# Optimization experiments

Hardware: AMD Instinct MI355X
Metric: run time of the kernel (lower is better)

The kernel has to match this reference:

```python
import jax, jax.numpy as jnp
import numpy as np

C = 3.0e8
WAVE_LAMBDA = 0.0038
PI = float(np.pi)


def _grid(size, resolution, x_val):
    edge_left = [-i for i in range(1, size, 2)][::-1]
    edge_right = [i for i in range(1, size, 2)]
    edge = edge_left + edge_right
    if size % 2 == 1:
        edge = [i for i in range(-(size - 1), size, 2)]
    edge = np.array(edge, dtype=np.float32) * resolution / 2.0
    wx, wy = np.meshgrid(edge, edge)
    wz = np.zeros((size, size), dtype=np.float32)
    pos = np.stack((wz, wx, wy), 2).reshape(size * size, 3).astype(np.float32)
    pos[:, 0] = x_val
    return pos


def setup_inputs() -> dict:
    key = jax.random.key(0)
    k1, k2, k3 = jax.random.split(key, 3)
    lam = WAVE_LAMBDA
    f = np.arange(77e9, 81e9 + 1e9, 1e9, dtype=np.float32)  # [5]
    tx = np.array([[0, -8 * lam, 0], [0, -6 * lam, 0], [0, -4 * lam, 0], [0, -2 * lam, 0],
                   [0, 0, 0], [0, 2 * lam, 0], [0, 4 * lam, 0], [0, 6 * lam, 0], [0, 8 * lam, 0],
                   [0, -2.5 * lam, -3 * lam], [0, -3.0 * lam, -2 * lam], [0, -3.5 * lam, -0.5 * lam]],
                  dtype=np.float32)  # [12,3]
    rx = np.array([[0, -16 * lam, -0.066], [0, -15.5 * lam, -0.066], [0, -15 * lam, -0.066],
                   [0, -14.5 * lam, -0.066], [0, -10.5 * lam, -0.066], [0, -10 * lam, -0.066],
                   [0, -9.5 * lam, -0.066], [0, -9 * lam, -0.066], [0, 7 * lam, -0.066],
                   [0, 7.5 * lam, -0.066], [0, 8 * lam, -0.066], [0, 8.5 * lam, -0.066],
                   [0, 9 * lam, -0.066], [0, 9.5 * lam, -0.066], [0, 10 * lam, -0.066],
                   [0, 10.5 * lam, -0.066]], dtype=np.float32)  # [16,3]
    meta = _grid(60, 0.0015, 0.1)     # [3600,3]
    scene = _grid(20, 0.0015, 0.3)    # [400,3] (resolution reassigned to 0.0015 in torch init)
    # trainable params
    meta_theta = jax.random.uniform(k1, (3600, 1), jnp.float32,
                                    minval=-PI, maxval=20 * PI / 180.0)
    w = jax.random.normal(k2, (5, 6, 12), jnp.float32)
    T = jax.random.normal(k3, (400, 128), jnp.float32)
    return {"T": T, "w": w, "meta_theta": meta_theta, "f": jnp.asarray(f),
            "tx_positions": jnp.asarray(tx), "rx_positions": jnp.asarray(rx),
            "meta_positions": jnp.asarray(meta), "scene_positions": jnp.asarray(scene)}


def _channel(locs_start, locs_end, f):
    # pairwise distance [Ns,Ne], then complex channel [F,Ns,Ne]
    d = jnp.linalg.norm(locs_start[:, None, :] - locs_end[None, :, :], axis=2)
    return (0.001 / d ** 2) * jnp.exp(-1j * 2 * PI * f[:, None, None] * d / C)


def reference(T, w, meta_theta, f, tx_positions, rx_positions, meta_positions, scene_positions):
    theta = jnp.clip(meta_theta, -PI, 20 * PI / 180.0)[:, 0]   # [M]
    phase = jnp.exp(1j * theta)                                # [M]
    pri = jnp.exp(1j * w)                                      # [F,6,Tx]
    H1 = _channel(tx_positions, meta_positions, f)             # [F,Tx,M]
    H2 = _channel(meta_positions, scene_positions, f)          # [F,M,S]
    H3 = _channel(scene_positions, meta_positions, f)          # [F,S,M]
    H4 = _channel(meta_positions, rx_positions, f)             # [F,M,Rx]
    A = jnp.einsum('fkt,ftm->fkm', pri, H1)                    # [F,6,M]
    A = A * phase[None, None, :]
    A = jnp.einsum('fkm,fms->fks', A, H2)                      # [F,6,S]
    # diag_embed(A) @ H3  ==  per-row scaling of H3 (no dense SxS diag needed)
    A = A[..., None] * H3[:, None, :, :]                       # [F,6,S,M]
    A = A * phase[None, None, None, :]
    A = jnp.einsum('fksm,fmr->fksr', A, H4)                    # [F,6,S,Rx]
    A = jnp.transpose(A, (3, 0, 1, 2))                         # [Rx,F,6,S]
    A = jnp.tile(A, (1, 1, 12, 1))                             # [Rx,F,72,S]
    A = A.reshape(-1, A.shape[3])                              # [Rx*F*72, S]
    T_complex = T.astype(jnp.complex64)
    mic_data = A @ T_complex                                   # [Rx*F*72, B]
    s_A = jnp.concatenate([A.real, A.imag], axis=0)            # [2*Rx*F*72, S]
    s_mic = jnp.concatenate([mic_data.real, mic_data.imag], axis=0)[..., None]
    return (s_A, s_mic)
```

## Files before the change

### kernel.cpp

```cpp
#include <hip/hip_runtime.h>
#include <hip/hip_bf16.h>
#include <math.h>

#define F_N 5
#define K_N 6
#define T_N 12
#define M_N 3600
#define S_N 400
#define R_N 16
#define B_N 128

#define PI_F 3.14159265358979f
#define CLIP_HI 0.3490658503988659f
#define NEG_TWO_PI_OVER_C (-6.283185307179586f / 3.0e8f)

#define SA_BASE   0
#define MIC_BASE  4608000

#define NK 113
#define KP (NK * 32)
#define W_ELEMS  (5 * 48 * KP)
#define H_ELEMS  (5 * 800 * KP)
#define C_ELEMS  (4 * 5 * 48 * 800)
#define WS_NEED  ((size_t)(W_ELEMS + H_ELEMS) * 2 + (size_t)C_ELEMS * 4)

typedef __attribute__((ext_vector_type(8))) short bf16x8;
typedef __attribute__((ext_vector_type(4))) float f32x4;

__device__ __forceinline__ void fast_sincos(float x, float* s, float* c) {
    float r = x * 0.15915494309189535f;
    r -= floorf(r);
    *s = __builtin_amdgcn_sinf(r);
    *c = __builtin_amdgcn_cosf(r);
}


__global__ __launch_bounds__(256) void stage_kernel(
    const float* __restrict__ w, const float* __restrict__ meta_theta,
    const float* __restrict__ fin, const float* __restrict__ txp,
    const float* __restrict__ rxp, const float* __restrict__ metap,
    const float* __restrict__ scenep,
    __hip_bfloat16* __restrict__ Wbf, __hip_bfloat16* __restrict__ Hbf)
{
    const int tid = threadIdx.x;
    const int blk = blockIdx.x;

    if (blk < 75) {
        __shared__ float pri[K_N * T_N * 2];
        __shared__ float txs[T_N * 3];
        __shared__ float rxs[R_N * 3];
        const int f = blk / 15;
        const int mblk = blk % 15;

        if (tid < K_N * T_N) {
            float sv, cv; fast_sincos(w[f * (K_N * T_N) + tid], &sv, &cv);
            pri[tid * 2] = cv; pri[tid * 2 + 1] = sv;
        }
        if (tid >= 64 && tid < 64 + T_N * 3) txs[tid - 64] = txp[tid - 64];
        if (tid >= 128 && tid < 128 + R_N * 3) rxs[tid - 128] = rxp[tid - 128];
        __syncthreads();

        const int m = mblk * 256 + tid;
        if (m >= KP) return;
        __hip_bfloat16* wb = Wbf + ((size_t)(f * NK + (m >> 5)) * 48) * 32 + (m & 31);

        if (m >= M_N) {
            for (int row = 0; row < 48; ++row) wb[row * 32] = __float2bfloat16(0.f);
            return;
        }

        const float px = metap[m * 3 + 0];
        const float py = metap[m * 3 + 1];
        const float pz = metap[m * 3 + 2];
        const float coef = NEG_TWO_PI_OVER_C * fin[f];

        float th = meta_theta[m];
        th = fminf(fmaxf(th, -PI_F), CLIP_HI);
        float phs, phc; fast_sincos(th, &phs, &phc);

        float hre[T_N], him[T_N];
#pragma unroll
        for (int t = 0; t < T_N; ++t) {
            float dx = txs[t * 3 + 0] - px, dy = txs[t * 3 + 1] - py, dz = txs[t * 3 + 2] - pz;
            float d = sqrtf(dx * dx + dy * dy + dz * dz);
            float amp = 1e-3f / (d * d);
            float sv, cv; fast_sincos(coef * d, &sv, &cv);
            hre[t] = amp * cv; him[t] = amp * sv;
        }
#pragma unroll
        for (int k = 0; k < K_N; ++k) {
            float ar = 0.f, ai = 0.f;
#pragma unroll
            for (int t = 0; t < T_N; ++t) {
                float pr = pri[(k * T_N + t) * 2], pim = pri[(k * T_N + t) * 2 + 1];
                ar += pr * hre[t] - pim * him[t];
                ai += pr * him[t] + pim * hre[t];
            }
            wb[k * 32]        = __float2bfloat16(ar * phc - ai * phs);
            wb[(22 + k) * 32] = __float2bfloat16(ar * phs + ai * phc);
        }
#pragma unroll
        for (int r = 0; r < R_N; ++r) {
            float dx = rxs[r * 3 + 0] - px, dy = rxs[r * 3 + 1] - py, dz = rxs[r * 3 + 2] - pz;
            float d = sqrtf(dx * dx + dy * dy + dz * dz);
            float amp = 1e-3f / (d * d);
            float sv, cv; fast_sincos(coef * d, &sv, &cv);
            float cr = amp * cv, ci = amp * sv;
            wb[(6 + r) * 32]  = __float2bfloat16(cr * phc - ci * phs);
            wb[(28 + r) * 32] = __float2bfloat16(cr * phs + ci * phc);
        }
#pragma unroll
        for (int row = 44; row < 48; ++row) wb[row * 32] = __float2bfloat16(0.f);
    } else {
        const int q = blk - 75;
        const int f = q / S_N;
        const int s = q % S_N;
        const float coef = NEG_TWO_PI_OVER_C * fin[f];
        const float sx = scenep[s * 3 + 0];
        const float sy = scenep[s * 3 + 1];
        const float sz = scenep[s * 3 + 2];

        for (int m = tid; m < KP; m += 256) {
            float re = 0.f, im = 0.f;
            if (m < M_N) {
                float px = metap[m * 3 + 0], py = metap[m * 3 + 1], pz = metap[m * 3 + 2];
                float dx = px - sx, dy = py - sy, dz = pz - sz;
                float d = sqrtf(dx * dx + dy * dy + dz * dz);
                float amp = 1e-3f / (d * d);
                float sv, cv; fast_sincos(coef * d, &sv, &cv);
                re = amp * cv; im = amp * sv;
            }
            size_t idx = ((size_t)(f * NK + (m >> 5)) * 800 + s) * 32 + (m & 31);
            Hbf[idx] = __float2bfloat16(re);
            Hbf[idx + 400 * 32] = __float2bfloat16(im);
        }
    }
}

__global__ __launch_bounds__(128) void gemm_kernel(
    const ushort* __restrict__ Wbf, const ushort* __restrict__ Hbf,
    float* __restrict__ Cp)
{
    const int blk = blockIdx.x;
    const int f = blk / 100;
    const int rem = blk % 100;
    const int nblk = rem / 4;
    const int ksp = rem % 4;
    const int wave = threadIdx.x >> 6;
    const int lane = threadIdx.x & 63;
    const int quad = lane >> 4;
    const int l16 = lane & 15;

    const int n = nblk * 32 + wave * 16 + l16;
    const int kbeg = (ksp == 0) ? 0 : (29 + 28 * (ksp - 1));
    const int kcnt = (ksp == 0) ? 29 : 28;

    f32x4 acc0 = {0.f, 0.f, 0.f, 0.f};
    f32x4 acc1 = {0.f, 0.f, 0.f, 0.f};
    f32x4 acc2 = {0.f, 0.f, 0.f, 0.f};

    for (int kk = 0; kk < kcnt; ++kk) {
        const int kb = kbeg + kk;
        bf16x8 b  = *(const bf16x8*)(Hbf + ((size_t)(f * NK + kb) * 800 + n) * 32 + quad * 8);
        const ushort* wbase = Wbf + ((size_t)(f * NK + kb) * 48) * 32 + quad * 8;
        bf16x8 a0 = *(const bf16x8*)(wbase + (size_t)l16 * 32);
        bf16x8 a1 = *(const bf16x8*)(wbase + (size_t)(16 + l16) * 32);
        bf16x8 a2 = *(const bf16x8*)(wbase + (size_t)(32 + l16) * 32);
        acc0 = __builtin_amdgcn_mfma_f32_16x16x32_bf16(a0, b, acc0, 0, 0, 0);
        acc1 = __builtin_amdgcn_mfma_f32_16x16x32_bf16(a1, b, acc1, 0, 0, 0);
        acc2 = __builtin_amdgcn_mfma_f32_16x16x32_bf16(a2, b, acc2, 0, 0, 0);
    }

    float* cb = Cp + ((size_t)(ksp * 5 + f) * 48) * 800;
#pragma unroll
    for (int i = 0; i < 4; ++i) {
        int row = quad * 4 + i;
        cb[(size_t)row * 800 + n]        = acc0[i];
        cb[(size_t)(16 + row) * 800 + n] = acc1[i];
        cb[(size_t)(32 + row) * 800 + n] = acc2[i];
    }
}

__device__ __forceinline__ void combineC(const float* __restrict__ Cp, int f, int row,
                                         int s, float* re, float* im) {
    float r = 0.f, i = 0.f;
#pragma unroll
    for (int p = 0; p < 4; ++p) {
        const float* c = Cp + ((size_t)(p * 5 + f) * 48) * 800;
        r += c[(size_t)row * 800 + s]       - c[(size_t)(22 + row) * 800 + 400 + s];
        i += c[(size_t)row * 800 + 400 + s] + c[(size_t)(22 + row) * 800 + s];
    }
    *re = r; *im = i;
}

#define SA_BLOCKS 750
__global__ __launch_bounds__(256) void epilogue2_kernel(
    const float* __restrict__ Cp, const float* __restrict__ T,
    float* __restrict__ out)
{
    __shared__ float cre[S_N], cim[S_N];
    __shared__ float pR[256], pI[256];
    const int tid = threadIdx.x;
    const int blk = blockIdx.x;

    if (blk < SA_BLOCKS) {
        int i = blk * 256 + tid;
        int s = i % S_N; int rest = i / S_N;
        int k = rest % K_N; rest /= K_N;
        int f = rest % F_N; int r = rest / F_N;

        float ar, ai, br, bi;
        combineC(Cp, f, k, s, &ar, &ai);
        combineC(Cp, f, 6 + r, s, &br, &bi);
        float cr = ar * br - ai * bi;
        float ci = ar * bi + ai * br;

        int base = (r * F_N + f) * 72;
#pragma unroll
        for (int j = 0; j < 12; ++j) {
            int row = base + j * K_N + k;
            out[SA_BASE + (size_t)row * S_N + s] = cr;
            out[SA_BASE + (size_t)(5760 + row) * S_N + s] = ci;
        }
    } else {
        int bk = blk - SA_BLOCKS;
        int k = bk % K_N;
        int f = (bk / K_N) % F_N;
        int r = bk / (K_N * F_N);

        for (int s = tid; s < S_N; s += 256) {
            float ar, ai, br, bi;
            combineC(Cp, f, k, s, &ar, &ai);
            combineC(Cp, f, 6 + r, s, &br, &bi);
            cre[s] = ar * br - ai * bi;
            cim[s] = ar * bi + ai * br;
        }
        __syncthreads();

        const int b = tid & 127;
        const int hs = tid >> 7;
        float accR = 0.f, accI = 0.f;
        const int sBeg = hs * 200, sEnd = sBeg + 200;
#pragma unroll 4
        for (int s = sBeg; s < sEnd; ++s) {
            float tv = T[s * B_N + b];
            accR += cre[s] * tv;
            accI += cim[s] * tv;
        }
        pR[tid] = accR; pI[tid] = accI;
        __syncthreads();
        if (tid < 128) {
            accR = pR[tid] + pR[tid + 128];
            accI = pI[tid] + pI[tid + 128];
            int base = (r * F_N + f) * 72;
#pragma unroll
            for (int j = 0; j < 12; ++j) {
                int row = base + j * K_N + k;
                out[MIC_BASE + (size_t)row * B_N + b] = accR;
                out[MIC_BASE + (size_t)(5760 + row) * B_N + b] = accI;
            }
        }
    }
}

__global__ __launch_bounds__(256) void prep_kernel(
    const float* __restrict__ w, const float* __restrict__ meta_theta,
    const float* __restrict__ fin, const float* __restrict__ txp,
    const float* __restrict__ rxp, const float* __restrict__ metap,
    float* __restrict__ A1, float* __restrict__ H4p)
{
    __shared__ float pri[K_N * T_N * 2];
    __shared__ float txs[T_N * 3];
    __shared__ float rxs[R_N * 3];
    const int tid = threadIdx.x;
    const int f = blockIdx.x / 15;
    const int mblk = blockIdx.x % 15;

    if (tid < K_N * T_N) {
        float sv, cv; fast_sincos(w[f * (K_N * T_N) + tid], &sv, &cv);
        pri[tid * 2] = cv; pri[tid * 2 + 1] = sv;
    }
    if (tid >= 64 && tid < 64 + T_N * 3) txs[tid - 64] = txp[tid - 64];
    if (tid >= 128 && tid < 128 + R_N * 3) rxs[tid - 128] = rxp[tid - 128];
    __syncthreads();

    const int m = mblk * 256 + tid;
    if (m >= M_N) return;

    const float px = metap[m * 3 + 0];
    const float py = metap[m * 3 + 1];
    const float pz = metap[m * 3 + 2];
    const float coef = NEG_TWO_PI_OVER_C * fin[f];

    float th = meta_theta[m];
    th = fminf(fmaxf(th, -PI_F), CLIP_HI);
    float phs, phc; fast_sincos(th, &phs, &phc);

    float hre[T_N], him[T_N];
#pragma unroll
    for (int t = 0; t < T_N; ++t) {
        float dx = txs[t * 3 + 0] - px, dy = txs[t * 3 + 1] - py, dz = txs[t * 3 + 2] - pz;
        float d = sqrtf(dx * dx + dy * dy + dz * dz);
        float amp = 1e-3f / (d * d);
        float sv, cv; fast_sincos(coef * d, &sv, &cv);
        hre[t] = amp * cv; him[t] = amp * sv;
    }
    float* a1 = A1 + ((size_t)f * M_N + m) * (K_N * 2);
#pragma unroll
    for (int k = 0; k < K_N; ++k) {
        float ar = 0.f, ai = 0.f;
#pragma unroll
        for (int t = 0; t < T_N; ++t) {
            float pr = pri[(k * T_N + t) * 2], pim = pri[(k * T_N + t) * 2 + 1];
            ar += pr * hre[t] - pim * him[t];
            ai += pr * him[t] + pim * hre[t];
        }
        a1[k * 2]     = ar * phc - ai * phs;
        a1[k * 2 + 1] = ar * phs + ai * phc;
    }
    float* h4 = H4p + ((size_t)f * M_N + m) * (R_N * 2);
#pragma unroll
    for (int r = 0; r < R_N; ++r) {
        float dx = rxs[r * 3 + 0] - px, dy = rxs[r * 3 + 1] - py, dz = rxs[r * 3 + 2] - pz;
        float d = sqrtf(dx * dx + dy * dy + dz * dz);
        float amp = 1e-3f / (d * d);
        float sv, cv; fast_sincos(coef * d, &sv, &cv);
        float cr = amp * cv, ci = amp * sv;
        h4[r * 2]     = cr * phc - ci * phs;
        h4[r * 2 + 1] = cr * phs + ci * phc;
    }
}

__global__ __launch_bounds__(256, 2) void main_kernel(
    const float* __restrict__ fin, const float* __restrict__ metap,
    const float* __restrict__ scenep, const float* __restrict__ A1,
    const float* __restrict__ H4p, float* __restrict__ A2, float* __restrict__ Bm)
{
    const int f = blockIdx.x / 200;
    const int sq = blockIdx.x % 200;
    const int s0 = 2 * sq, s1 = s0 + 1;
    const int tid = threadIdx.x;

    const float coef = NEG_TWO_PI_OVER_C * fin[f];
    const float sx0 = scenep[s0 * 3], sy0 = scenep[s0 * 3 + 1], sz0 = scenep[s0 * 3 + 2];
    const float sx1 = scenep[s1 * 3], sy1 = scenep[s1 * 3 + 1], sz1 = scenep[s1 * 3 + 2];

    float acc[88];
#pragma unroll
    for (int i = 0; i < 88; ++i) acc[i] = 0.f;

    const float4* a1base = (const float4*)(A1 + (size_t)f * M_N * (K_N * 2));
    const float4* h4base = (const float4*)(H4p + (size_t)f * M_N * (R_N * 2));

    for (int m = tid; m < M_N; m += 256) {
        float px = metap[m * 3 + 0], py = metap[m * 3 + 1], pz = metap[m * 3 + 2];
        float dx0 = px - sx0, dy0 = py - sy0, dz0 = pz - sz0;
        float d0 = sqrtf(dx0 * dx0 + dy0 * dy0 + dz0 * dz0);
        float dx1 = px - sx1, dy1 = py - sy1, dz1 = pz - sz1;
        float d1 = sqrtf(dx1 * dx1 + dy1 * dy1 + dz1 * dz1);
        float sv0, cv0, sv1, cv1;
        fast_sincos(coef * d0, &sv0, &cv0);
        fast_sincos(coef * d1, &sv1, &cv1);
        float amp0 = 1e-3f / (d0 * d0), amp1 = 1e-3f / (d1 * d1);
        float h2r0 = amp0 * cv0, h2i0 = amp0 * sv0;
        float h2r1 = amp1 * cv1, h2i1 = amp1 * sv1;

        const float4* a1 = a1base + (size_t)m * 3;
#pragma unroll
        for (int q = 0; q < 3; ++q) {
            float4 v = a1[q];
            acc[4 * q + 0] += v.x * h2r0 - v.y * h2i0;
            acc[4 * q + 1] += v.x * h2i0 + v.y * h2r0;
            acc[4 * q + 2] += v.z * h2r0 - v.w * h2i0;
            acc[4 * q + 3] += v.z * h2i0 + v.w * h2r0;
            acc[44 + 4 * q + 0] += v.x * h2r1 - v.y * h2i1;
            acc[44 + 4 * q + 1] += v.x * h2i1 + v.y * h2r1;
            acc[44 + 4 * q + 2] += v.z * h2r1 - v.w * h2i1;
            acc[44 + 4 * q + 3] += v.z * h2i1 + v.w * h2r1;
        }
        const float4* h4 = h4base + (size_t)m * 8;
#pragma unroll
        for (int q = 0; q < 8; ++q) {
            float4 v = h4[q];
            acc[12 + 4 * q + 0] += v.x * h2r0 - v.y * h2i0;
            acc[12 + 4 * q + 1] += v.x * h2i0 + v.y * h2r0;
            acc[12 + 4 * q + 2] += v.z * h2r0 - v.w * h2i0;
            acc[12 + 4 * q + 3] += v.z * h2i0 + v.w * h2r0;
            acc[56 + 4 * q + 0] += v.x * h2r1 - v.y * h2i1;
            acc[56 + 4 * q + 1] += v.x * h2i1 + v.y * h2r1;
            acc[56 + 4 * q + 2] += v.z * h2r1 - v.w * h2i1;
            acc[56 + 4 * q + 3] += v.z * h2i1 + v.w * h2r1;
        }
    }

#pragma unroll
    for (int off = 32; off > 0; off >>= 1) {
#pragma unroll
        for (int i = 0; i < 88; ++i) acc[i] += __shfl_down(acc[i], off);
    }
    __shared__ float red[4][88];
    const int wave = tid >> 6, lane = tid & 63;
    if (lane == 0) {
#pragma unroll
        for (int i = 0; i < 88; ++i) red[wave][i] = acc[i];
    }
    __syncthreads();
    if (tid < 88) {
        float v = red[0][tid] + red[1][tid] + red[2][tid] + red[3][tid];
        int half = tid / 44, slot = tid - 44 * half;
        int s = half ? s1 : s0;
        if (slot < 12) {
            int k = slot >> 1, c = slot & 1;
            A2[(((size_t)f * K_N + k) * S_N + s) * 2 + c] = v;
        } else {
            int j = slot - 12; int r = j >> 1, c = j & 1;
            Bm[(((size_t)f * S_N + s) * R_N + r) * 2 + c] = v;
        }
    }
}

__global__ __launch_bounds__(256) void epilogue_kernel(
    const float* __restrict__ A2, const float* __restrict__ Bm,
    const float* __restrict__ T, float* __restrict__ out)
{
    __shared__ float cre[S_N], cim[S_N];
    __shared__ float pR[256], pI[256];
    const int tid = threadIdx.x;
    const int blk = blockIdx.x;

    if (blk < SA_BLOCKS) {
        int i = blk * 256 + tid;
        int s = i % S_N; int rest = i / S_N;
        int k = rest % K_N; rest /= K_N;
        int f = rest % F_N; int r = rest / F_N;

        float ar = A2[((f * K_N + k) * S_N + s) * 2];
        float ai = A2[((f * K_N + k) * S_N + s) * 2 + 1];
        float br = Bm[((f * S_N + s) * R_N + r) * 2];
        float bi = Bm[((f * S_N + s) * R_N + r) * 2 + 1];
        float cr = ar * br - ai * bi;
        float ci = ar * bi + ai * br;

        int base = (r * F_N + f) * 72;
#pragma unroll
        for (int j = 0; j < 12; ++j) {
            int row = base + j * K_N + k;
            out[SA_BASE + (size_t)row * S_N + s] = cr;
            out[SA_BASE + (size_t)(5760 + row) * S_N + s] = ci;
        }
    } else {
        int bk = blk - SA_BLOCKS;
        int k = bk % K_N;
        int f = (bk / K_N) % F_N;
        int r = bk / (K_N * F_N);

        for (int s = tid; s < S_N; s += 256) {
            float ar = A2[((f * K_N + k) * S_N + s) * 2];
            float ai = A2[((f * K_N + k) * S_N + s) * 2 + 1];
            float br = Bm[((f * S_N + s) * R_N + r) * 2];
            float bi = Bm[((f * S_N + s) * R_N + r) * 2 + 1];
            cre[s] = ar * br - ai * bi;
            cim[s] = ar * bi + ai * br;
        }
        __syncthreads();

        const int b = tid & 127;
        const int hs = tid >> 7;
        float accR = 0.f, accI = 0.f;
        const int sBeg = hs * 200, sEnd = sBeg + 200;
#pragma unroll 4
        for (int s = sBeg; s < sEnd; ++s) {
            float tv = T[s * B_N + b];
            accR += cre[s] * tv;
            accI += cim[s] * tv;
        }
        pR[tid] = accR; pI[tid] = accI;
        __syncthreads();
        if (tid < 128) {
            accR = pR[tid] + pR[tid + 128];
            accI = pI[tid] + pI[tid + 128];
            int base = (r * F_N + f) * 72;
#pragma unroll
            for (int j = 0; j < 12; ++j) {
                int row = base + j * K_N + k;
                out[MIC_BASE + (size_t)row * B_N + b] = accR;
                out[MIC_BASE + (size_t)(5760 + row) * B_N + b] = accI;
            }
        }
    }
}

extern "C" void kernel_launch(void* const* d_in, const int* in_sizes, int n_in,
                              void* d_out, int out_size, void* d_ws, size_t ws_size,
                              hipStream_t stream) {
    const float* T  = (const float*)d_in[0];
    const float* w  = (const float*)d_in[1];
    const float* th = (const float*)d_in[2];
    const float* fr = (const float*)d_in[3];
    const float* tx = (const float*)d_in[4];
    const float* rx = (const float*)d_in[5];
    const float* mp = (const float*)d_in[6];
    const float* sp = (const float*)d_in[7];

    float* out = (float*)d_out;

    if (ws_size >= WS_NEED) {
        __hip_bfloat16* Wbf = (__hip_bfloat16*)d_ws;
        __hip_bfloat16* Hbf = Wbf + W_ELEMS;
        float* Cp = (float*)(Hbf + H_ELEMS);

        stage_kernel<<<75 + 2000, 256, 0, stream>>>(w, th, fr, tx, rx, mp, sp, Wbf, Hbf);
        gemm_kernel<<<500, 128, 0, stream>>>((const ushort*)Wbf, (const ushort*)Hbf, Cp);
        epilogue2_kernel<<<SA_BLOCKS + 480, 256, 0, stream>>>(Cp, T, out);
    } else {
        float* ws  = (float*)d_ws;
        float* A1  = ws;
        float* H4p = ws + 216000;
        float* A2  = ws + 792000;
        float* Bm  = ws + 816000;

        prep_kernel<<<75, 256, 0, stream>>>(w, th, fr, tx, rx, mp, A1, H4p);
        main_kernel<<<F_N * 200, 256, 0, stream>>>(fr, mp, sp, A1, H4p, A2, Bm);
        epilogue_kernel<<<SA_BLOCKS + 480, 256, 0, stream>>>(A2, Bm, T, out);
    }
}
```

Before: 122.8 us.

## Compute scene-meta channel on the fly inside GEMM instead of materializing it

The stage kernel no longer builds the bf16 H matrix (scene×meta channel, real and imaginary parts) in workspace. Instead, each GEMM lane computes its B-fragment values (distance, amplitude, sin or cos) directly from the positions before issuing the MFMAs. This removes roughly 2000 stage blocks and a large global write and read round-trip. In exchange the GEMM loop does transcendental math per element, and the real and imaginary halves each recompute the shared distance work. The GEMM grid is only 500 blocks, so compute latency may not be hidden.

```diff
diff --git a/kernel.cpp b/kernel.cpp
--- a/kernel.cpp
+++ b/kernel.cpp
@@ -13,6 +13,7 @@
 #define PI_F 3.14159265358979f
 #define CLIP_HI 0.3490658503988659f
 #define NEG_TWO_PI_OVER_C (-6.283185307179586f / 3.0e8f)
+#define INV_TWO_PI 0.15915494309189535f
 
 #define SA_BASE   0
 #define MIC_BASE  4608000
@@ -20,18 +21,23 @@
 #define NK 113
 #define KP (NK * 32)
 #define W_ELEMS  (5 * 48 * KP)
-#define H_ELEMS  (5 * 800 * KP)
 #define C_ELEMS  (4 * 5 * 48 * 800)
-#define WS_NEED  ((size_t)(W_ELEMS + H_ELEMS) * 2 + (size_t)C_ELEMS * 4)
+#define WS_NEED  ((size_t)W_ELEMS * 2 + (size_t)C_ELEMS * 4)
 
 typedef __attribute__((ext_vector_type(8))) short bf16x8;
 typedef __attribute__((ext_vector_type(4))) float f32x4;
 
 __device__ __forceinline__ void fast_sincos(float x, float* s, float* c) {
-    float r = x * 0.15915494309189535f;
+    float r = x * INV_TWO_PI;
     r -= floorf(r);
     *s = __builtin_amdgcn_sinf(r);
     *c = __builtin_amdgcn_cosf(r);
+}
+
+__device__ __forceinline__ ushort f2bf(float v) {
+    __hip_bfloat16 h = __float2bfloat16(v);
+    union { __hip_bfloat16 h; ushort u; } cv; cv.h = h;
+    return cv.u;
 }
 
 
@@ -39,106 +45,79 @@
     const float* __restrict__ w, const float* __restrict__ meta_theta,
     const float* __restrict__ fin, const float* __restrict__ txp,
     const float* __restrict__ rxp, const float* __restrict__ metap,
-    const float* __restrict__ scenep,
-    __hip_bfloat16* __restrict__ Wbf, __hip_bfloat16* __restrict__ Hbf)
+    __hip_bfloat16* __restrict__ Wbf)
 {
+    __shared__ float pri[K_N * T_N * 2];
+    __shared__ float txs[T_N * 3];
+    __shared__ float rxs[R_N * 3];
     const int tid = threadIdx.x;
-    const int blk = blockIdx.x;
-
-    if (blk < 75) {
-        __shared__ float pri[K_N * T_N * 2];
-        __shared__ float txs[T_N * 3];
-        __shared__ float rxs[R_N * 3];
-        const int f = blk / 15;
-        const int mblk = blk % 15;
-
-        if (tid < K_N * T_N) {
-            float sv, cv; fast_sincos(w[f * (K_N * T_N) + tid], &sv, &cv);
-            pri[tid * 2] = cv; pri[tid * 2 + 1] = sv;
-        }
-        if (tid >= 64 && tid < 64 + T_N * 3) txs[tid - 64] = txp[tid - 64];
-        if (tid >= 128 && tid < 128 + R_N * 3) rxs[tid - 128] = rxp[tid - 128];
-        __syncthreads();
-
-        const int m = mblk * 256 + tid;
-        if (m >= KP) return;
-        __hip_bfloat16* wb = Wbf + ((size_t)(f * NK + (m >> 5)) * 48) * 32 + (m & 31);
-
-        if (m >= M_N) {
-            for (int row = 0; row < 48; ++row) wb[row * 32] = __float2bfloat16(0.f);
-            return;
-        }
-
-        const float px = metap[m * 3 + 0];
-        const float py = metap[m * 3 + 1];
-        const float pz = metap[m * 3 + 2];
-        const float coef = NEG_TWO_PI_OVER_C * fin[f];
-
-        float th = meta_theta[m];
-        th = fminf(fmaxf(th, -PI_F), CLIP_HI);
-        float phs, phc; fast_sincos(th, &phs, &phc);
-
-        float hre[T_N], him[T_N];
+    const int f = blockIdx.x / 15;
+    const int mblk = blockIdx.x % 15;
+
+    if (tid < K_N * T_N) {
+        float sv, cv; fast_sincos(w[f * (K_N * T_N) + tid], &sv, &cv);
+        pri[tid * 2] = cv; pri[tid * 2 + 1] = sv;
+    }
+    if (tid >= 64 && tid < 64 + T_N * 3) txs[tid - 64] = txp[tid - 64];
+    if (tid >= 128 && tid < 128 + R_N * 3) rxs[tid - 128] = rxp[tid - 128];
+    __syncthreads();
+
+    const int m = mblk * 256 + tid;
+    if (m >= KP) return;
+    __hip_bfloat16* wb = Wbf + ((size_t)(f * NK + (m >> 5)) * 48) * 32 + (m & 31);
+
+    if (m >= M_N) {
+        for (int row = 0; row < 48; ++row) wb[row * 32] = __float2bfloat16(0.f);
+        return;
+    }
+
+    const float px = metap[m * 3 + 0];
+    const float py = metap[m * 3 + 1];
+    const float pz = metap[m * 3 + 2];
+    const float coef = NEG_TWO_PI_OVER_C * fin[f];
+
+    float th = meta_theta[m];
+    th = fminf(fmaxf(th, -PI_F), CLIP_HI);
+    float phs, phc; fast_sincos(th, &phs, &phc);
+
+    float hre[T_N], him[T_N];
+#pragma unroll
+    for (int t = 0; t < T_N; ++t) {
+        float dx = txs[t * 3 + 0] - px, dy = txs[t * 3 + 1] - py, dz = txs[t * 3 + 2] - pz;
+        float d = sqrtf(dx * dx + dy * dy + dz * dz);
+        float amp = 1e-3f / (d * d);
+        float sv, cv; fast_sincos(coef * d, &sv, &cv);
+        hre[t] = amp * cv; him[t] = amp * sv;
+    }
+#pragma unroll
+    for (int k = 0; k < K_N; ++k) {
+        float ar = 0.f, ai = 0.f;
 #pragma unroll
         for (int t = 0; t < T_N; ++t) {
-            float dx = txs[t * 3 + 0] - px, dy = txs[t * 3 + 1] - py, dz = txs[t * 3 + 2] - pz;
-            float d = sqrtf(dx * dx + dy * dy + dz * dz);
-            float amp = 1e-3f / (d * d);
-            float sv, cv; fast_sincos(coef * d, &sv, &cv);
-            hre[t] = amp * cv; him[t] = amp * sv;
-        }
-#pragma unroll
-        for (int k = 0; k < K_N; ++k) {
-            float ar = 0.f, ai = 0.f;
-#pragma unroll
-            for (int t = 0; t < T_N; ++t) {
-                float pr = pri[(k * T_N + t) * 2], pim = pri[(k * T_N + t) * 2 + 1];
-                ar += pr * hre[t] - pim * him[t];
-                ai += pr * him[t] + pim * hre[t];
-            }
-            wb[k * 32]        = __float2bfloat16(ar * phc - ai * phs);
-            wb[(22 + k) * 32] = __float2bfloat16(ar * phs + ai * phc);
-        }
-#pragma unroll
-        for (int r = 0; r < R_N; ++r) {
-            float dx = rxs[r * 3 + 0] - px, dy = rxs[r * 3 + 1] - py, dz = rxs[r * 3 + 2] - pz;
-            float d = sqrtf(dx * dx + dy * dy + dz * dz);
-            float amp = 1e-3f / (d * d);
-            float sv, cv; fast_sincos(coef * d, &sv, &cv);
-            float cr = amp * cv, ci = amp * sv;
-            wb[(6 + r) * 32]  = __float2bfloat16(cr * phc - ci * phs);
-            wb[(28 + r) * 32] = __float2bfloat16(cr * phs + ci * phc);
-        }
-#pragma unroll
-        for (int row = 44; row < 48; ++row) wb[row * 32] = __float2bfloat16(0.f);
-    } else {
-        const int q = blk - 75;
-        const int f = q / S_N;
-        const int s = q % S_N;
-        const float coef = NEG_TWO_PI_OVER_C * fin[f];
-        const float sx = scenep[s * 3 + 0];
-        const float sy = scenep[s * 3 + 1];
-        const float sz = scenep[s * 3 + 2];
-
-        for (int m = tid; m < KP; m += 256) {
-            float re = 0.f, im = 0.f;
-            if (m < M_N) {
-                float px = metap[m * 3 + 0], py = metap[m * 3 + 1], pz = metap[m * 3 + 2];
-                float dx = px - sx, dy = py - sy, dz = pz - sz;
-                float d = sqrtf(dx * dx + dy * dy + dz * dz);
-                float amp = 1e-3f / (d * d);
-                float sv, cv; fast_sincos(coef * d, &sv, &cv);
-                re = amp * cv; im = amp * sv;
-            }
-            size_t idx = ((size_t)(f * NK + (m >> 5)) * 800 + s) * 32 + (m & 31);
-            Hbf[idx] = __float2bfloat16(re);
-            Hbf[idx + 400 * 32] = __float2bfloat16(im);
-        }
-    }
+            float pr = pri[(k * T_N + t) * 2], pim = pri[(k * T_N + t) * 2 + 1];
+            ar += pr * hre[t] - pim * him[t];
+            ai += pr * him[t] + pim * hre[t];
+        }
+        wb[k * 32]        = __float2bfloat16(ar * phc - ai * phs);
+        wb[(22 + k) * 32] = __float2bfloat16(ar * phs + ai * phc);
+    }
+#pragma unroll
+    for (int r = 0; r < R_N; ++r) {
+        float dx = rxs[r * 3 + 0] - px, dy = rxs[r * 3 + 1] - py, dz = rxs[r * 3 + 2] - pz;
+        float d = sqrtf(dx * dx + dy * dy + dz * dz);
+        float amp = 1e-3f / (d * d);
+        float sv, cv; fast_sincos(coef * d, &sv, &cv);
+        float cr = amp * cv, ci = amp * sv;
+        wb[(6 + r) * 32]  = __float2bfloat16(cr * phc - ci * phs);
+        wb[(28 + r) * 32] = __float2bfloat16(cr * phs + ci * phc);
+    }
+#pragma unroll
+    for (int row = 44; row < 48; ++row) wb[row * 32] = __float2bfloat16(0.f);
 }
 
 __global__ __launch_bounds__(128) void gemm_kernel(
-    const ushort* __restrict__ Wbf, const ushort* __restrict__ Hbf,
+    const ushort* __restrict__ Wbf, const float* __restrict__ fin,
+    const float* __restrict__ metap, const float* __restrict__ scenep,
     float* __restrict__ Cp)
 {
     const int blk = blockIdx.x;
@@ -152,8 +131,15 @@
     const int l16 = lane & 15;
 
     const int n = nblk * 32 + wave * 16 + l16;
+    const int isIm = (n >= 400);
+    const int s = isIm ? (n - 400) : n;
     const int kbeg = (ksp == 0) ? 0 : (29 + 28 * (ksp - 1));
     const int kcnt = (ksp == 0) ? 29 : 28;
+
+    const float coef = NEG_TWO_PI_OVER_C * fin[f];
+    const float sx = scenep[s * 3 + 0];
+    const float sy = scenep[s * 3 + 1];
+    const float sz = scenep[s * 3 + 2];
 
     f32x4 acc0 = {0.f, 0.f, 0.f, 0.f};
     f32x4 acc1 = {0.f, 0.f, 0.f, 0.f};
@@ -161,14 +147,34 @@
 
     for (int kk = 0; kk < kcnt; ++kk) {
         const int kb = kbeg + kk;
-        bf16x8 b  = *(const bf16x8*)(Hbf + ((size_t)(f * NK + kb) * 800 + n) * 32 + quad * 8);
+        const int m0 = kb * 32 + quad * 8;
+
+        union { ushort u[8]; bf16x8 v; } bu;
+#pragma unroll
+        for (int j = 0; j < 8; ++j) {
+            const int m = m0 + j;
+            float val = 0.f;
+            if (m < M_N) {
+                float dx = metap[m * 3 + 0] - sx;
+                float dy = metap[m * 3 + 1] - sy;
+                float dz = metap[m * 3 + 2] - sz;
+                float d = sqrtf(dx * dx + dy * dy + dz * dz);
+                float amp = 1e-3f / (d * d);
+                float r = coef * d * INV_TWO_PI;
+                r -= floorf(r);
+                float tr = isIm ? __builtin_amdgcn_sinf(r) : __builtin_amdgcn_cosf(r);
+                val = amp * tr;
+            }
+            bu.u[j] = f2bf(val);
+        }
+
         const ushort* wbase = Wbf + ((size_t)(f * NK + kb) * 48) * 32 + quad * 8;
         bf16x8 a0 = *(const bf16x8*)(wbase + (size_t)l16 * 32);
         bf16x8 a1 = *(const bf16x8*)(wbase + (size_t)(16 + l16) * 32);
         bf16x8 a2 = *(const bf16x8*)(wbase + (size_t)(32 + l16) * 32);
-        acc0 = __builtin_amdgcn_mfma_f32_16x16x32_bf16(a0, b, acc0, 0, 0, 0);
-        acc1 = __builtin_amdgcn_mfma_f32_16x16x32_bf16(a1, b, acc1, 0, 0, 0);
-        acc2 = __builtin_amdgcn_mfma_f32_16x16x32_bf16(a2, b, acc2, 0, 0, 0);
+        acc0 = __builtin_amdgcn_mfma_f32_16x16x32_bf16(a0, bu.v, acc0, 0, 0, 0);
+        acc1 = __builtin_amdgcn_mfma_f32_16x16x32_bf16(a1, bu.v, acc1, 0, 0, 0);
+        acc2 = __builtin_amdgcn_mfma_f32_16x16x32_bf16(a2, bu.v, acc2, 0, 0, 0);
     }
 
     float* cb = Cp + ((size_t)(ksp * 5 + f) * 48) * 800;
@@ -506,11 +512,10 @@
 
     if (ws_size >= WS_NEED) {
         __hip_bfloat16* Wbf = (__hip_bfloat16*)d_ws;
-        __hip_bfloat16* Hbf = Wbf + W_ELEMS;
-        float* Cp = (float*)(Hbf + H_ELEMS);
-
-        stage_kernel<<<75 + 2000, 256, 0, stream>>>(w, th, fr, tx, rx, mp, sp, Wbf, Hbf);
-        gemm_kernel<<<500, 128, 0, stream>>>((const ushort*)Wbf, (const ushort*)Hbf, Cp);
+        float* Cp = (float*)((char*)d_ws + (size_t)W_ELEMS * 2);
+
+        stage_kernel<<<75, 256, 0, stream>>>(w, th, fr, tx, rx, mp, Wbf);
+        gemm_kernel<<<500, 128, 0, stream>>>((const ushort*)Wbf, fr, mp, sp, Cp);
         epilogue2_kernel<<<SA_BLOCKS + 480, 256, 0, stream>>>(Cp, T, out);
     } else {
         float* ws  = (float*)d_ws;
```

Result: slower. 164.3 us (+33.8%).
